# Performance work log

Measured on AMD Instinct MI355X. Metric: run time of the kernel, lower is better.

The kernel has to match this reference:

```python
import jax, jax.numpy as jnp
import numpy as np
import math

SEQ = 16384      # total ragged tokens
DIM = 1280       # vision hidden size
HEADS = 16
HDIM = DIM // HEADS  # 80
NSEG = 16        # number of segments (images); equal lengths of 1024


def rotate_half(x):
    x1, x2 = jnp.split(x, 2, axis=-1)
    return jnp.concatenate([-x2, x1], axis=-1)


def setup_inputs() -> dict:
    key = jax.random.key(0)
    ks = jax.random.split(key, 6)
    hidden_states = jax.random.normal(ks[0], (SEQ, DIM), dtype=jnp.float32)
    # rotary tables over the full head_dim (Qwen vision style: freqs duplicated)
    inv_freq = 1.0 / (10000.0 ** (jnp.arange(0, HDIM, 2, dtype=jnp.float32) / HDIM))
    pos = jnp.arange(SEQ, dtype=jnp.float32)
    freqs = jnp.outer(pos, inv_freq)                      # [S, HDIM/2]
    emb = jnp.concatenate([freqs, freqs], axis=-1)        # [S, HDIM]
    cos, sin = jnp.cos(emb), jnp.sin(emb)
    w_qkv = jax.random.normal(ks[1], (3 * DIM, DIM), dtype=jnp.float32) * 0.02
    b_qkv = jax.random.normal(ks[2], (3 * DIM,), dtype=jnp.float32) * 0.02
    w_proj = jax.random.normal(ks[3], (DIM, DIM), dtype=jnp.float32) * 0.02
    b_proj = jax.random.normal(ks[4], (DIM,), dtype=jnp.float32) * 0.02
    cu_seqlens = jnp.arange(NSEG + 1, dtype=jnp.int32) * (SEQ // NSEG)
    return {"hidden_states": hidden_states, "cos": cos, "sin": sin,
            "w_qkv": w_qkv, "b_qkv": b_qkv, "w_proj": w_proj, "b_proj": b_proj,
            "cu_seqlens": cu_seqlens}


def reference(hidden_states, cos, sin, w_qkv, b_qkv, w_proj, b_proj, cu_seqlens):
    S, D = hidden_states.shape
    hd = cos.shape[-1]
    nh = D // hd
    nseg = cu_seqlens.shape[0] - 1
    L = S // nseg  # equal segment lengths (matches cu_seqlens built in setup)

    qkv = hidden_states @ w_qkv.T + b_qkv                 # [S, 3D]
    qkv = qkv.reshape(S, 3, nh, hd)
    q, k, v = qkv[:, 0], qkv[:, 1], qkv[:, 2]             # [S, H, hd]

    # rotary (computed in float32, as in the original)
    c = cos[:, None, :]
    s = sin[:, None, :]
    q = q * c + rotate_half(q) * s
    k = k * c + rotate_half(k) * s

    # block-diagonal attention: reshape ragged-equal segments into a batch dim
    qs = q.reshape(nseg, L, nh, hd)
    ks = k.reshape(nseg, L, nh, hd)
    vs = v.reshape(nseg, L, nh, hd)

    scale = 1.0 / math.sqrt(hd)
    scores = jnp.einsum('bqhd,bkhd->bhqk', qs, ks) * scale   # [nseg, H, L, L]
    probs = jax.nn.softmax(scores, axis=-1)
    out = jnp.einsum('bhqk,bkhd->bqhd', probs, vs)           # [nseg, L, H, hd]
    out = out.reshape(S, D)
    return out @ w_proj.T + b_proj
```

## Files before the change

### kernel.cpp

```cpp
#include <hip/hip_runtime.h>

#define SEQ 16384
#define DIM 1280
#define NH 16
#define HD 80
#define NSEG 16
#define SEGL 1024

typedef __attribute__((ext_vector_type(8))) short bf16x8;
typedef __attribute__((ext_vector_type(4))) float f32x4;

__device__ inline unsigned short f2bf(float f){
  unsigned int x = __builtin_bit_cast(unsigned int, f);
  unsigned int r = (x + 0x7FFFu + ((x >> 16) & 1u)) >> 16;
  return (unsigned short)r;
}
__device__ inline float bf2f(unsigned short u){
  unsigned int x = ((unsigned int)u) << 16;
  return __builtin_bit_cast(float, x);
}
__device__ inline int cvtpk_bf16(float lo, float hi){
  int r;
  asm("v_cvt_pk_bf16_f32 %0, %1, %2" : "=v"(r) : "v"(lo), "v"(hi));
  return r;
}

__device__ inline void gload16(const unsigned short* g, unsigned short* l){
  __builtin_amdgcn_global_load_lds((const __attribute__((address_space(1))) void*)g,
                                   (__attribute__((address_space(3))) void*)l, 16, 0, 0);
}

__global__ __launch_bounds__(256) void pack_bf16_kernel(const float* __restrict__ src,
                                                        unsigned short* __restrict__ dst, int n4){
  int i = blockIdx.x * 256 + threadIdx.x;
  if (i >= n4) return;
  float4 v = ((const float4*)src)[i];
  ushort4 o;
  o.x = f2bf(v.x); o.y = f2bf(v.y); o.z = f2bf(v.z); o.w = f2bf(v.w);
  ((ushort4*)dst)[i] = o;
}

template<int EPI>
__global__ __launch_bounds__(512, 2) void gemm256_kernel(const unsigned short* __restrict__ A,
    const unsigned short* __restrict__ B, const float* __restrict__ bias,
    void* __restrict__ Cout, unsigned short* __restrict__ Vtg, int M, int N, int K){
  __shared__ __attribute__((aligned(16))) unsigned short As[2][16384];
  __shared__ __attribute__((aligned(16))) unsigned short Bs[2][16384];
  const int nwg = gridDim.x;
  int bid = blockIdx.x;
  int swz = (bid & 7) * (nwg >> 3) + (bid >> 3);
  const int ntn = N >> 8;
  const int tm = (swz / ntn) << 8;
  const int tn = (swz % ntn) << 8;
  const int tid = threadIdx.x;
  const int wid = tid >> 6, l = tid & 63;
  const int lr = l & 15, lh = l >> 4;
  const int wrM = (wid >> 2) << 7;
  const int wcN = (wid & 3) << 6;
  const int NITER = K >> 7;

  const int srow = wid*8 + (l >> 3);
  const int scol = ((l & 7) ^ (l >> 3)) << 3;
  const int sldsu = wid << 9;

  const unsigned short* Ag = A + (size_t)tm * K;
  const unsigned short* Bg = B + (size_t)tn * K;

  const int ck0 = (lh*8) ^ ((l & 7) << 3);
  const int ck1 = (32 + lh*8) ^ ((l & 7) << 3);
  const int raA = (wrM + lr) << 6;
  const int raB = (wcN + lr) << 6;

  f32x4 zf = {0.f,0.f,0.f,0.f};
  f32x4 acc[8][4];
  #pragma unroll
  for (int i=0;i<8;i++)
    #pragma unroll
    for (int j=0;j<4;j++) acc[i][j] = zf;

#define STAGE_A(tile, h, q) gload16(Ag + (size_t)((h)*128 + (q)*64 + srow)*K + ((tile)<<6) + scol, \
                                    &As[(tile)&1][(h)*8192 + (q)*4096 + sldsu])
#define STAGE_B(tile, h, q) gload16(Bg + (size_t)((h)*128 + (q)*64 + srow)*K + ((tile)<<6) + scol, \
                                    &Bs[(tile)&1][(h)*8192 + (q)*4096 + sldsu])
#define RD_A(b, MOFF) \
  _Pragma("unroll") \
  for (int mi=0; mi<4; ++mi){ \
    a[0][mi] = *(const bf16x8*)&As[b][raA + ((MOFF)+mi)*1024 + ck0]; \
    a[1][mi] = *(const bf16x8*)&As[b][raA + ((MOFF)+mi)*1024 + ck1]; }
#define RD_B(b, NOFF, BREG) \
  _Pragma("unroll") \
  for (int nj=0; nj<2; ++nj){ \
    BREG[0][nj] = *(const bf16x8*)&Bs[b][raB + ((NOFF)+nj)*1024 + ck0]; \
    BREG[1][nj] = *(const bf16x8*)&Bs[b][raB + ((NOFF)+nj)*1024 + ck1]; }
#define BAR() __builtin_amdgcn_s_barrier();
#define QMFMA(MB, NB, BREG) \
  __builtin_amdgcn_s_setprio(1); \
  _Pragma("unroll") \
  for (int mi=0; mi<4; ++mi){ \
    _Pragma("unroll") \
    for (int nj=0; nj<2; ++nj){ \
      acc[(MB)+mi][(NB)+nj] = __builtin_amdgcn_mfma_f32_16x16x32_bf16(a[0][mi], BREG[0][nj], acc[(MB)+mi][(NB)+nj], 0,0,0); \
      acc[(MB)+mi][(NB)+nj] = __builtin_amdgcn_mfma_f32_16x16x32_bf16(a[1][mi], BREG[1][nj], acc[(MB)+mi][(NB)+nj], 0,0,0); \
    } \
  } \
  __builtin_amdgcn_s_setprio(0); \
  __builtin_amdgcn_s_barrier();

  #pragma unroll
  for (int q=0;q<2;q++){ STAGE_A(0,0,q); }
  #pragma unroll
  for (int q=0;q<2;q++){ STAGE_A(0,1,q); }
  #pragma unroll
  for (int q=0;q<2;q++){ STAGE_B(0,0,q); }
  #pragma unroll
  for (int q=0;q<2;q++){ STAGE_B(0,1,q); }
  #pragma unroll
  for (int q=0;q<2;q++){ STAGE_B(1,0,q); }
  #pragma unroll
  for (int q=0;q<2;q++){ STAGE_B(1,1,q); }
  #pragma unroll
  for (int q=0;q<2;q++){ STAGE_A(1,0,q); }
  #pragma unroll
  for (int q=0;q<2;q++){ STAGE_A(1,1,q); }
  asm volatile("s_waitcnt vmcnt(8)" ::: "memory");
  __builtin_amdgcn_s_barrier();

  for (int i=0; i<NITER; ++i){
    const int T = 2*i;
    const bool st = (i+1 < NITER);
    bf16x8 a[2][4], bx[2][2], by[2][2];

    RD_B(0, 0, bx); RD_A(0, 0);
    BAR(); QMFMA(0, 0, bx);

    RD_B(0, 2, by);
    BAR(); QMFMA(0, 2, by);

    RD_A(0, 4);
    if (st){ STAGE_B(T+2, 0, 0); STAGE_B(T+2, 0, 1); }
    BAR(); QMFMA(4, 2, by);

    if (st){
      STAGE_B(T+2, 1, 0); STAGE_B(T+2, 1, 1);
      STAGE_A(T+2, 0, 0); STAGE_A(T+2, 0, 1);
      asm volatile("s_waitcnt vmcnt(6)" ::: "memory");
    } else {
      asm volatile("s_waitcnt vmcnt(0)" ::: "memory");
    }
    BAR(); QMFMA(4, 0, bx);

    RD_B(1, 0, bx); RD_A(1, 0);
    if (st){ STAGE_A(T+2, 1, 0); STAGE_A(T+2, 1, 1); }
    BAR(); QMFMA(0, 0, bx);

    RD_B(1, 2, by);
    BAR(); QMFMA(0, 2, by);

    RD_A(1, 4);
    if (st){ STAGE_B(T+3, 0, 0); STAGE_B(T+3, 0, 1); STAGE_B(T+3, 1, 0); STAGE_B(T+3, 1, 1); }
    BAR(); QMFMA(4, 2, by);

    if (st){
      STAGE_A(T+3, 0, 0); STAGE_A(T+3, 0, 1); STAGE_A(T+3, 1, 0); STAGE_A(T+3, 1, 1);
      asm volatile("s_waitcnt vmcnt(8)" ::: "memory");
    }
    BAR(); QMFMA(4, 0, bx);
  }

#undef STAGE_A
#undef STAGE_B
#undef RD_A
#undef RD_B
#undef BAR
#undef QMFMA

  #pragma unroll
  for (int nj=0;nj<4;nj++){
    int col = tn + wcN + nj*16 + lr;
    float bv = bias[col];
    if (EPI == 0){
      int which = col / DIM;
      int rem = col - which*DIM;
      int hh = rem / HD;
      int d = rem - hh*HD;
      if (which == 2){
        unsigned short* Vd = Vtg + ((size_t)hh * HD + d) * SEQ;
        #pragma unroll
        for (int mi=0;mi<8;mi++){
          int row0 = tm + wrM + mi*16 + lh*4;
          int g = (row0 >> 2) & 15;
          int pg = ((g>>3)<<3) + ((g&3)<<1) + ((g>>2)&1);
          int s = (row0 & ~63) + pg*4;
          unsigned int w0 = (unsigned int)cvtpk_bf16(acc[mi][nj][0]+bv, acc[mi][nj][1]+bv);
          unsigned int w1 = (unsigned int)cvtpk_bf16(acc[mi][nj][2]+bv, acc[mi][nj][3]+bv);
          uint2 ov = {w0, w1};
          *(uint2*)(Vd + s) = ov;
        }
      } else {
        unsigned short* Q = (unsigned short*)Cout;
        size_t base = (size_t)(which*NH + hh) * SEQ;
        #pragma unroll
        for (int mi=0;mi<8;mi++){
          #pragma unroll
          for (int r=0;r<4;r++){
            int row = tm + wrM + mi*16 + lh*4 + r;
            Q[(base + row)*HD + d] = f2bf(acc[mi][nj][r] + bv);
          }
        }
      }
    } else {
      float* C = (float*)Cout;
      #pragma unroll
      for (int mi=0;mi<8;mi++){
        #pragma unroll
        for (int r=0;r<4;r++){
          int row = tm + wrM + mi*16 + lh*4 + r;
          C[(size_t)row*N + col] = acc[mi][nj][r] + bv;
        }
      }
    }
  }
}

__global__ __launch_bounds__(256) void rope_kernel(unsigned short* __restrict__ QKV,
    const float* __restrict__ cosb, const float* __restrict__ sinb){
  unsigned int gid = blockIdx.x * 256 + threadIdx.x;
  int pd = gid % 40;
  unsigned int row = gid / 40;
  int s = row % SEQ;
  float f = (row < (unsigned)(NH*SEQ)) ? (0.111803398874989485f * 1.4426950408889634f) : 1.0f;
  unsigned short* p = QKV + (size_t)row * HD;
  float c  = cosb[s*HD + pd];
  float sn = sinb[s*HD + pd];
  float x1 = bf2f(p[pd]);
  float x2 = bf2f(p[pd+40]);
  p[pd]    = f2bf((x1*c - x2*sn)*f);
  p[pd+40] = f2bf((x2*c + x1*sn)*f);
}

__global__ __launch_bounds__(512) void attn_kernel(const unsigned short* __restrict__ QKV,
                                                   const unsigned short* __restrict__ Vt,
                                                   unsigned short* __restrict__ AO){
  int bid = blockIdx.x;
  int qt  = (bid >> 3) & 7;
  int g   = (bid & 7) * 32 + (bid >> 6);
  int h   = g & 15;
  int seg = g >> 4;
  int tid = threadIdx.x, wid = tid >> 6, l = tid & 63;
  int lr = l & 15, lh = l >> 4;
  const unsigned short* Qb = QKV + (size_t)(0*NH + h) * SEQ * HD;
  const unsigned short* Kb = QKV + (size_t)(1*NH + h) * SEQ * HD;
  const unsigned short* Vtb = Vt + (size_t)h * HD * SEQ;
  int q0 = seg*SEGL + qt*128;
  __shared__ __attribute__((aligned(16))) unsigned short Ksm[5152];
  __shared__ __attribute__((aligned(16))) unsigned short Vtsm[5120];
  bf16x8 qf[3];
  {
    const unsigned short* qp = Qb + (size_t)(q0 + wid*16 + lr) * HD;
    #pragma unroll
    for (int c=0;c<3;c++){
      int d0 = c*32 + lh*8;
      bf16x8 z = {0,0,0,0,0,0,0,0};
      qf[c] = (d0 < HD) ? *(const bf16x8*)(qp + d0) : z;
    }
  }
  f32x4 zf = {0.f,0.f,0.f,0.f};
  f32x4 o[5];
  #pragma unroll
  for (int dt=0;dt<5;dt++) o[dt] = zf;
  float m = -1e30f, lsum = 0.f;
  for (int kt=0; kt<16; kt++){
    int k0 = seg*SEGL + kt*64;
    const unsigned short* Ksrc = Kb + (size_t)k0 * HD;
    gload16(Ksrc + (wid*64 + l)*8, &Ksm[wid*512]);
    if (wid < 2){
      gload16(Ksrc + (512 + wid*64 + l)*8, &Ksm[4096 + wid*512]);
    } else {
      int uv = (wid-2)*64 + l;
      int d = uv >> 3, c16 = uv & 7;
      gload16(Vtb + (size_t)d*SEQ + k0 + ((c16 ^ (d & 7)) << 3), &Vtsm[(wid-2)*512]);
    }
    if (wid < 4){
      int uv = 384 + wid*64 + l;
      int d = uv >> 3, c16 = uv & 7;
      gload16(Vtb + (size_t)d*SEQ + k0 + ((c16 ^ (d & 7)) << 3), &Vtsm[3072 + wid*512]);
    }
    __syncthreads();
    f32x4 s[4];
    #pragma unroll
    for (int n=0;n<4;n++) s[n] = zf;
    #pragma unroll
    for (int c=0;c<3;c++){
      #pragma unroll
      for (int n=0;n<4;n++){
        bf16x8 kf = *(const bf16x8*)&Ksm[(n*16+lr)*80 + c*32 + lh*8];
        s[n] = __builtin_amdgcn_mfma_f32_16x16x32_bf16(kf, qf[c], s[n], 0,0,0);
      }
    }
    float pm = s[0][0];
    #pragma unroll
    for (int n=0;n<4;n++)
      #pragma unroll
      for (int r=0;r<4;r++) pm = fmaxf(pm, s[n][r]);
    pm = fmaxf(pm, __shfl_xor(pm, 16));
    pm = fmaxf(pm, __shfl_xor(pm, 32));
    if (!__all(pm <= m + 8.f)){
      float mn = fmaxf(m, pm);
      float corr = exp2f(m - mn);
      lsum *= corr;
      #pragma unroll
      for (int dt=0;dt<5;dt++)
        #pragma unroll
        for (int r=0;r<4;r++) o[dt][r] *= corr;
      m = mn;
    }
    float rs = 0.f;
    #pragma unroll
    for (int n=0;n<4;n++)
      #pragma unroll
      for (int r=0;r<4;r++){
        float p = exp2f(s[n][r] - m);
        s[n][r] = p;
        rs += p;
      }
    rs += __shfl_xor(rs, 16);
    rs += __shfl_xor(rs, 32);
    lsum += rs;
    int w[8];
    #pragma unroll
    for (int n=0;n<4;n++){
      w[2*n]   = cvtpk_bf16(s[n][0], s[n][1]);
      w[2*n+1] = cvtpk_bf16(s[n][2], s[n][3]);
    }
    #pragma unroll
    for (int kc=0;kc<2;kc++){
      union { bf16x8 v; int u[4]; } pf;
      pf.u[0] = w[4*kc+0]; pf.u[1] = w[4*kc+1];
      pf.u[2] = w[4*kc+2]; pf.u[3] = w[4*kc+3];
      #pragma unroll
      for (int dt=0;dt<5;dt++){
        int row = dt*16 + lr;
        bf16x8 vf = *(const bf16x8*)&Vtsm[row*64 + ((kc*32 + lh*8) ^ ((lr & 7) << 3))];
        o[dt] = __builtin_amdgcn_mfma_f32_16x16x32_bf16(vf, pf.v, o[dt], 0,0,0);
      }
    }
    __syncthreads();
  }
  float inv = 1.0f / lsum;
  int qrow = q0 + wid*16 + lr;
  unsigned short* op = AO + (size_t)qrow*DIM + h*HD;
  #pragma unroll
  for (int dt=0;dt<5;dt++){
    unsigned int w0 = (unsigned int)cvtpk_bf16(o[dt][0]*inv, o[dt][1]*inv);
    unsigned int w1 = (unsigned int)cvtpk_bf16(o[dt][2]*inv, o[dt][3]*inv);
    uint2 ov = {w0, w1};
    *(uint2*)(op + dt*16 + lh*4) = ov;
  }
}

extern "C" void kernel_launch(void* const* d_in, const int* in_sizes, int n_in,
                              void* d_out, int out_size, void* d_ws, size_t ws_size,
                              hipStream_t stream){
  const float* hs    = (const float*)d_in[0];
  const float* cosb  = (const float*)d_in[1];
  const float* sinb  = (const float*)d_in[2];
  const float* wqkv  = (const float*)d_in[3];
  const float* bqkv  = (const float*)d_in[4];
  const float* wproj = (const float*)d_in[5];
  const float* bproj = (const float*)d_in[6];
  float* out = (float*)d_out;

  unsigned short* Abf    = (unsigned short*)d_ws;
  unsigned short* Wqkvb  = Abf + (size_t)SEQ*DIM;
  unsigned short* Wprojb = Wqkvb + (size_t)3*DIM*DIM;
  unsigned short* QKVb   = Wprojb + (size_t)DIM*DIM;
  unsigned short* Vtb    = QKVb + (size_t)3*SEQ*DIM;
  unsigned short* AObf   = Abf;

  pack_bf16_kernel<<<(SEQ*DIM/4)/256, 256, 0, stream>>>(hs, Abf, SEQ*DIM/4);
  pack_bf16_kernel<<<(3*DIM*DIM/4)/256, 256, 0, stream>>>(wqkv, Wqkvb, 3*DIM*DIM/4);
  pack_bf16_kernel<<<(DIM*DIM/4)/256, 256, 0, stream>>>(wproj, Wprojb, DIM*DIM/4);

  gemm256_kernel<0><<<(SEQ/256)*((3*DIM)/256), 512, 0, stream>>>(Abf, Wqkvb, bqkv,
                                                                 (void*)QKVb, Vtb, SEQ, 3*DIM, DIM);

  rope_kernel<<<(2*NH*SEQ*40)/256, 256, 0, stream>>>(QKVb, cosb, sinb);

  attn_kernel<<<NSEG*NH*(SEGL/128), 512, 0, stream>>>(QKVb, Vtb, AObf);

  gemm256_kernel<1><<<(SEQ/256)*(DIM/256), 512, 0, stream>>>(AObf, Wprojb, bproj,
                                                             (void*)out, nullptr, SEQ, DIM, DIM);
}
```

Baseline: 467.0 us.

## Double-buffer K/V tiles in attention with async prefetch and MFMA priority

Splits the K and V^T shared-memory tiles into two buffers and issues the global-to-LDS loads for the next key tile before computing the current one. Explicit vmcnt waits and raw barriers replace __syncthreads, so the load latency can overlap with the MFMA and softmax work. s_setprio is raised around the MFMA blocks to favour matrix issue across waves. The cost is doubled LDS use, which may lower occupancy, and the hand-counted vmcnt values must match the per-wave load counts or reads will see stale data.

New measurement: 473.4 us. Within noise of the previous version (+1.4%).

```diff
diff --git a/kernel.cpp b/kernel.cpp
--- a/kernel.cpp
+++ b/kernel.cpp
@@ -252,8 +252,9 @@
   const unsigned short* Kb = QKV + (size_t)(1*NH + h) * SEQ * HD;
   const unsigned short* Vtb = Vt + (size_t)h * HD * SEQ;
   int q0 = seg*SEGL + qt*128;
-  __shared__ __attribute__((aligned(16))) unsigned short Ksm[5152];
-  __shared__ __attribute__((aligned(16))) unsigned short Vtsm[5120];
+  __shared__ __attribute__((aligned(16))) unsigned short Ksm[2][5120];
+  __shared__ __attribute__((aligned(16))) unsigned short Vtsm[2][5120];
+
   bf16x8 qf[3];
   {
     const unsigned short* qp = Qb + (size_t)(q0 + wid*16 + lr) * HD;
@@ -264,39 +265,58 @@
       qf[c] = (d0 < HD) ? *(const bf16x8*)(qp + d0) : z;
     }
   }
+
+#define ATTN_STAGE(kt, buf) { \
+    int k0_ = seg*SEGL + (kt)*64; \
+    const unsigned short* Ksrc_ = Kb + (size_t)k0_ * HD; \
+    gload16(Ksrc_ + (wid*64 + l)*8, &Ksm[buf][wid*512]); \
+    if (wid < 2){ \
+      gload16(Ksrc_ + (512 + wid*64 + l)*8, &Ksm[buf][4096 + wid*512]); \
+    } else { \
+      int uv_ = (wid-2)*64 + l; \
+      int d_ = uv_ >> 3, c16_ = uv_ & 7; \
+      gload16(Vtb + (size_t)d_*SEQ + k0_ + ((c16_ ^ (d_ & 7)) << 3), &Vtsm[buf][(wid-2)*512]); \
+    } \
+    if (wid < 4){ \
+      int uv_ = 384 + wid*64 + l; \
+      int d_ = uv_ >> 3, c16_ = uv_ & 7; \
+      gload16(Vtb + (size_t)d_*SEQ + k0_ + ((c16_ ^ (d_ & 7)) << 3), &Vtsm[buf][3072 + wid*512]); \
+    } \
+  }
+
   f32x4 zf = {0.f,0.f,0.f,0.f};
   f32x4 o[5];
   #pragma unroll
   for (int dt=0;dt<5;dt++) o[dt] = zf;
   float m = -1e30f, lsum = 0.f;
+
+  ATTN_STAGE(0, 0);
+
   for (int kt=0; kt<16; kt++){
-    int k0 = seg*SEGL + kt*64;
-    const unsigned short* Ksrc = Kb + (size_t)k0 * HD;
-    gload16(Ksrc + (wid*64 + l)*8, &Ksm[wid*512]);
-    if (wid < 2){
-      gload16(Ksrc + (512 + wid*64 + l)*8, &Ksm[4096 + wid*512]);
+    int cb = kt & 1;
+    if (kt < 15){
+      ATTN_STAGE(kt+1, cb^1);
+      if (wid < 4){ asm volatile("s_waitcnt vmcnt(3)" ::: "memory"); }
+      else        { asm volatile("s_waitcnt vmcnt(2)" ::: "memory"); }
     } else {
-      int uv = (wid-2)*64 + l;
-      int d = uv >> 3, c16 = uv & 7;
-      gload16(Vtb + (size_t)d*SEQ + k0 + ((c16 ^ (d & 7)) << 3), &Vtsm[(wid-2)*512]);
-    }
-    if (wid < 4){
-      int uv = 384 + wid*64 + l;
-      int d = uv >> 3, c16 = uv & 7;
-      gload16(Vtb + (size_t)d*SEQ + k0 + ((c16 ^ (d & 7)) << 3), &Vtsm[3072 + wid*512]);
-    }
-    __syncthreads();
+      asm volatile("s_waitcnt vmcnt(0)" ::: "memory");
+    }
+    __builtin_amdgcn_s_barrier();
+
     f32x4 s[4];
     #pragma unroll
     for (int n=0;n<4;n++) s[n] = zf;
+    __builtin_amdgcn_s_setprio(1);
     #pragma unroll
     for (int c=0;c<3;c++){
       #pragma unroll
       for (int n=0;n<4;n++){
-        bf16x8 kf = *(const bf16x8*)&Ksm[(n*16+lr)*80 + c*32 + lh*8];
+        bf16x8 kf = *(const bf16x8*)&Ksm[cb][(n*16+lr)*80 + c*32 + lh*8];
         s[n] = __builtin_amdgcn_mfma_f32_16x16x32_bf16(kf, qf[c], s[n], 0,0,0);
       }
     }
+    __builtin_amdgcn_s_setprio(0);
+
     float pm = s[0][0];
     #pragma unroll
     for (int n=0;n<4;n++)
@@ -332,6 +352,7 @@
       w[2*n]   = cvtpk_bf16(s[n][0], s[n][1]);
       w[2*n+1] = cvtpk_bf16(s[n][2], s[n][3]);
     }
+    __builtin_amdgcn_s_setprio(1);
     #pragma unroll
     for (int kc=0;kc<2;kc++){
       union { bf16x8 v; int u[4]; } pf;
@@ -340,12 +361,15 @@
       #pragma unroll
       for (int dt=0;dt<5;dt++){
         int row = dt*16 + lr;
-        bf16x8 vf = *(const bf16x8*)&Vtsm[row*64 + ((kc*32 + lh*8) ^ ((lr & 7) << 3))];
+        bf16x8 vf = *(const bf16x8*)&Vtsm[cb][row*64 + ((kc*32 + lh*8) ^ ((lr & 7) << 3))];
         o[dt] = __builtin_amdgcn_mfma_f32_16x16x32_bf16(vf, pf.v, o[dt], 0,0,0);
       }
     }
-    __syncthreads();
-  }
+    __builtin_amdgcn_s_setprio(0);
+    __builtin_amdgcn_s_barrier();
+  }
+#undef ATTN_STAGE
+
   float inv = 1.0f / lsum;
   int qrow = q0 + wid*16 + lr;
   unsigned short* op = AO + (size_t)qrow*DIM + h*HD;
```
